# Kernel tuning notes

Hardware: AMD Instinct MI355X
Metric: run time of the kernel (lower is better)

The kernel has to match this reference:

```python
import jax, jax.numpy as jnp
import numpy as np


def setup_inputs() -> dict:
    key = jax.random.key(0)
    ks = jax.random.split(key, 5)
    B, C, H, W = 8, 64, 64, 64
    Ci = 32  # inter_channels = in_channels // 2
    s = 1.0 / np.sqrt(C)
    return {
        "x": jax.random.normal(ks[0], (B, C, H, W), jnp.float32),
        "Wg": jax.random.normal(ks[1], (Ci, C), jnp.float32) * s,
        "bg": jnp.zeros((Ci,), jnp.float32),
        "Wt": jax.random.normal(ks[2], (Ci, C), jnp.float32) * s,
        "bt": jnp.zeros((Ci,), jnp.float32),
        "Wp": jax.random.normal(ks[3], (Ci, C), jnp.float32) * s,
        "bp": jnp.zeros((Ci,), jnp.float32),
        "Ww": jax.random.normal(ks[4], (C, Ci), jnp.float32) * (1.0 / np.sqrt(Ci)),
        "bw": jnp.zeros((C,), jnp.float32),
    }


def _proj(x, Wc, bc):
    # 1x1 conv: (B,C,H,W) -> (B,O,H,W), then flatten spatial -> (B,O,N)
    b, c, h, w = x.shape
    y = jnp.einsum("oc,bchw->bohw", Wc, x) + bc[None, :, None, None]
    return y.reshape(b, Wc.shape[0], h * w)


def reference(x, Wg, bg, Wt, bt, Wp, bp, Ww, bw):
    b, c, h, w = x.shape
    g_x = _proj(x, Wg, bg).transpose(0, 2, 1)      # (B, N, Ci)
    theta_x = _proj(x, Wt, bt).transpose(0, 2, 1)  # (B, N, Ci)
    phi_x = _proj(x, Wp, bp)                        # (B, Ci, N)
    f = jnp.einsum("bnd,bdm->bnm", theta_x, phi_x)  # (B, N, N)
    f_div_C = jax.nn.softmax(f, axis=-1)
    y = jnp.einsum("bnm,bmd->bnd", f_div_C, g_x)    # (B, N, Ci)
    y = y.transpose(0, 2, 1).reshape(b, Wg.shape[0], h, w)
    W_y = jnp.einsum("od,bdhw->bohw", Ww, y) + bw[None, :, None, None]
    return W_y + x
```

## Files before the change

### kernel.cpp

```cpp
#include <hip/hip_runtime.h>
#include <hip/hip_bf16.h>
#include <cstdint>
#include <cstddef>

#define B_ 8
#define C_ 64
#define CI 32
#define N_ 4096
#define LOG2E 1.44269504088896340736f

typedef __attribute__((ext_vector_type(8))) short bf16x8;
typedef __attribute__((ext_vector_type(4))) float f32x4;

static __device__ __forceinline__ ushort f2bf(float x) {
  union { float f; uint32_t u; } v; v.f = x;
  uint32_t r = v.u + 0x7FFFu + ((v.u >> 16) & 1u);
  return (ushort)(r >> 16);
}

static __device__ __forceinline__ uint32_t cvt_pk_bf16(float lo, float hi) {
  uint32_t r;
  asm("v_cvt_pk_bf16_f32 %0, %1, %2" : "=v"(r) : "v"(lo), "v"(hi));
  return r;
}

__global__ __launch_bounds__(512) void proj_kernel(
    const float* __restrict__ x,
    const float* __restrict__ Wg, const float* __restrict__ bg,
    const float* __restrict__ Wt, const float* __restrict__ bt,
    const float* __restrict__ Wp, const float* __restrict__ bp,
    ushort* __restrict__ theta_t, ushort* __restrict__ phi_t,
    ushort* __restrict__ gmat)
{
  const int t = threadIdx.x;
  const int b = blockIdx.y;
  const int n = blockIdx.x * 64 + (t & 63);
  const int dg = __builtin_amdgcn_readfirstlane(t >> 6);
  const float* xb = x + ((size_t)b * C_) * N_ + n;
  const float* WtR = Wt + dg * 4 * C_;
  const float* WpR = Wp + dg * 4 * C_;
  const float* WgR = Wg + dg * 4 * C_;

  float at[4], ap[4], ag[4];
  #pragma unroll
  for (int i = 0; i < 4; ++i) {
    at[i] = bt[dg * 4 + i]; ap[i] = bp[dg * 4 + i]; ag[i] = bg[dg * 4 + i];
  }

  #pragma unroll
  for (int c0 = 0; c0 < C_; c0 += 4) {
    float xv[4];
    #pragma unroll
    for (int j = 0; j < 4; ++j) xv[j] = xb[(size_t)(c0 + j) * N_];
    #pragma unroll
    for (int i = 0; i < 4; ++i) {
      const float4 wt4 = *(const float4*)&WtR[i * C_ + c0];
      const float4 wp4 = *(const float4*)&WpR[i * C_ + c0];
      const float4 wg4 = *(const float4*)&WgR[i * C_ + c0];
      at[i] = fmaf(wt4.x, xv[0], at[i]); at[i] = fmaf(wt4.y, xv[1], at[i]);
      at[i] = fmaf(wt4.z, xv[2], at[i]); at[i] = fmaf(wt4.w, xv[3], at[i]);
      ap[i] = fmaf(wp4.x, xv[0], ap[i]); ap[i] = fmaf(wp4.y, xv[1], ap[i]);
      ap[i] = fmaf(wp4.z, xv[2], ap[i]); ap[i] = fmaf(wp4.w, xv[3], ap[i]);
      ag[i] = fmaf(wg4.x, xv[0], ag[i]); ag[i] = fmaf(wg4.y, xv[1], ag[i]);
      ag[i] = fmaf(wg4.z, xv[2], ag[i]); ag[i] = fmaf(wg4.w, xv[3], ag[i]);
    }
  }

  uint2 wt2, wp2;
  wt2.x = (uint32_t)f2bf(at[0] * LOG2E) | ((uint32_t)f2bf(at[1] * LOG2E) << 16);
  wt2.y = (uint32_t)f2bf(at[2] * LOG2E) | ((uint32_t)f2bf(at[3] * LOG2E) << 16);
  wp2.x = (uint32_t)f2bf(ap[0]) | ((uint32_t)f2bf(ap[1]) << 16);
  wp2.y = (uint32_t)f2bf(ap[2]) | ((uint32_t)f2bf(ap[3]) << 16);
  *(uint2*)(theta_t + ((size_t)(b * N_) + n) * CI + dg * 4) = wt2;
  *(uint2*)(phi_t   + ((size_t)(b * N_) + n) * CI + dg * 4) = wp2;
  #pragma unroll
  for (int i = 0; i < 4; ++i)
    gmat[((size_t)(b * CI) + dg * 4 + i) * N_ + n] = f2bf(ag[i]);
}

__global__ __launch_bounds__(512, 2) void attn_kernel(
    const ushort* __restrict__ theta_t,
    const ushort* __restrict__ phi_t,
    const ushort* __restrict__ gmat,
    const float* __restrict__ Ww, const float* __restrict__ bw,
    const float* __restrict__ x, float* __restrict__ out)
{
  __shared__ union {
    ushort pt[8][2][16 * 64];
    float  accS[4][32][64];
    float  yl[32 * 66];
  } Sh;
  __shared__ float mlS[4][8][64];
  __shared__ float WwL[C_ * CI];

  const int tid = threadIdx.x;
  const int lane = tid & 63;
  const int mh = tid >> 6;
  const int bid = blockIdx.x;
  const int b = bid & 7;
  const int n0 = (bid >> 3) * 64;
  const int g4 = lane >> 4;
  const int c16 = lane & 15;
  const int sw = (c16 & 7) << 4;

  #pragma unroll
  for (int i = 0; i < 4; ++i) WwL[tid + i * 512] = Ww[tid + i * 512];

  bf16x8 qfrag[4];
  #pragma unroll
  for (int s = 0; s < 4; ++s)
    qfrag[s] = *(const bf16x8*)(theta_t +
        ((size_t)(b * N_ + n0 + s * 16 + c16)) * CI + g4 * 8);

  f32x4 acc[4][2];
  f32x4 cinit[4];
  #pragma unroll
  for (int s = 0; s < 4; ++s) {
    acc[s][0] = (f32x4){0.f, 0.f, 0.f, 0.f};
    acc[s][1] = (f32x4){0.f, 0.f, 0.f, 0.f};
    cinit[s]  = (f32x4){0.f, 0.f, 0.f, 0.f};
  }
  float l_lane[4] = {0.f, 0.f, 0.f, 0.f};

  const int mq0 = mh * 512;
  const ushort* kbase = phi_t + ((size_t)(b * N_ + mq0 + c16)) * CI + g4 * 8;
  const ushort* vb0 = gmat + ((size_t)(b * CI + c16)) * N_ + mq0 + g4 * 8;
  const ushort* vb1 = vb0 + (size_t)16 * N_;

  char* pw[2][4]; const char* prd[2][2];
  #pragma unroll
  for (int pb = 0; pb < 2; ++pb) {
    #pragma unroll
    for (int mt = 0; mt < 4; ++mt)
      pw[pb][mt] = (char*)Sh.pt[mh][pb] + ((c16 * 128 + mt * 32 + g4 * 8) ^ sw);
    #pragma unroll
    for (int ks = 0; ks < 2; ++ks)
      prd[pb][ks] = (const char*)Sh.pt[mh][pb] +
                    ((c16 * 128 + ks * 64 + g4 * 16) ^ sw);
  }

  bf16x8 kf[4], kfn[4], vf0[2], vf1[2];
  #pragma unroll
  for (int mt = 0; mt < 4; ++mt)
    kfn[mt] = *(const bf16x8*)(kbase + (size_t)(mt * 16) * CI);

  const int NT = 8;
  for (int t = 0; t < NT; ++t) {
    #pragma unroll
    for (int mt = 0; mt < 4; ++mt) kf[mt] = kfn[mt];
    const int tn = (t + 1 < NT) ? t + 1 : t;
    #pragma unroll
    for (int mt = 0; mt < 4; ++mt)
      kfn[mt] = *(const bf16x8*)(kbase + (size_t)(tn * 64 + mt * 16) * CI);
    #pragma unroll
    for (int ks = 0; ks < 2; ++ks) {
      vf0[ks] = *(const bf16x8*)(vb0 + t * 64 + ks * 32);
      vf1[ks] = *(const bf16x8*)(vb1 + t * 64 + ks * 32);
    }

    #pragma unroll
    for (int s = 0; s < 4; ++s) {
      const int pb = s & 1;
      f32x4 f[4];
      #pragma unroll
      for (int mt = 0; mt < 4; ++mt)
        f[mt] = __builtin_amdgcn_mfma_f32_16x16x32_bf16(
            kf[mt], qfrag[s], cinit[s], 0, 0, 0);

      float pv[4][4];
      #pragma unroll
      for (int mt = 0; mt < 4; ++mt) {
        #pragma unroll
        for (int rr = 0; rr < 4; ++rr)
          pv[mt][rr] = __builtin_amdgcn_exp2f(f[mt][rr]);
        l_lane[s] += (pv[mt][0] + pv[mt][1]) + (pv[mt][2] + pv[mt][3]);
      }
      #pragma unroll
      for (int mt = 0; mt < 4; ++mt) {
        uint2 wv;
        wv.x = cvt_pk_bf16(pv[mt][0], pv[mt][1]);
        wv.y = cvt_pk_bf16(pv[mt][2], pv[mt][3]);
        *(uint2*)pw[pb][mt] = wv;
      }
      asm volatile("s_waitcnt lgkmcnt(0)" ::: "memory");

      #pragma unroll
      for (int ks = 0; ks < 2; ++ks) {
        const bf16x8 pfrag = *(const bf16x8*)prd[pb][ks];
        acc[s][0] = __builtin_amdgcn_mfma_f32_16x16x32_bf16(
            vf0[ks], pfrag, acc[s][0], 0, 0, 0);
        acc[s][1] = __builtin_amdgcn_mfma_f32_16x16x32_bf16(
            vf1[ks], pfrag, acc[s][1], 0, 0, 0);
      }

      if (__any(l_lane[s] > 0x1p40f)) {
        const float sc = 0x1p-64f;
        acc[s][0] *= sc; acc[s][1] *= sc; l_lane[s] *= sc;
        #pragma unroll
        for (int rr = 0; rr < 4; ++rr) cinit[s][rr] -= 64.f;
      }
    }
  }

  float m_run[4];
  #pragma unroll
  for (int s = 0; s < 4; ++s) {
    l_lane[s] += __shfl_xor(l_lane[s], 16);
    l_lane[s] += __shfl_xor(l_lane[s], 32);
    m_run[s] = -cinit[s][0];
  }

  #pragma unroll
  for (int r = 4; r >= 1; r >>= 1) {
    __syncthreads();
    if (mh >= r && mh < 2 * r) {
      float* ad = &Sh.accS[mh - r][0][0] + lane;
      float* md = &mlS[mh - r][0][0] + lane;
      #pragma unroll
      for (int s = 0; s < 4; ++s) {
        #pragma unroll
        for (int rr = 0; rr < 4; ++rr) {
          ad[(s * 8 + rr) * 64]     = acc[s][0][rr];
          ad[(s * 8 + 4 + rr) * 64] = acc[s][1][rr];
        }
        md[s * 64]       = m_run[s];
        md[(4 + s) * 64] = l_lane[s];
      }
    }
    __syncthreads();
    if (mh < r) {
      const float* as_ = &Sh.accS[mh][0][0] + lane;
      const float* ms_ = &mlS[mh][0][0] + lane;
      #pragma unroll
      for (int s = 0; s < 4; ++s) {
        const float mb = ms_[s * 64];
        const float lb = ms_[(4 + s) * 64];
        const float mM = fmaxf(m_run[s], mb);
        const float ea = __builtin_amdgcn_exp2f(m_run[s] - mM);
        const float eb = __builtin_amdgcn_exp2f(mb - mM);
        #pragma unroll
        for (int rr = 0; rr < 4; ++rr) {
          acc[s][0][rr] = acc[s][0][rr] * ea + as_[(s * 8 + rr) * 64] * eb;
          acc[s][1][rr] = acc[s][1][rr] * ea + as_[(s * 8 + 4 + rr) * 64] * eb;
        }
        l_lane[s] = l_lane[s] * ea + lb * eb;
        m_run[s] = mM;
      }
    }
  }
  __syncthreads();

  float* const Yl = Sh.yl;
  if (mh == 0) {
    #pragma unroll
    for (int s = 0; s < 4; ++s) {
      const float inv = 1.0f / l_lane[s];
      const int q = s * 16 + c16;
      #pragma unroll
      for (int rr = 0; rr < 4; ++rr) {
        Yl[(g4 * 4 + rr) * 66 + q]      = acc[s][0][rr] * inv;
        Yl[(16 + g4 * 4 + rr) * 66 + q] = acc[s][1][rr] * inv;
      }
    }
  }
  __syncthreads();

  const int nl = tid & 63;
  const int cg = tid >> 6;
  float oacc[8];
  #pragma unroll
  for (int i = 0; i < 8; ++i) oacc[i] = bw[cg * 8 + i];
  #pragma unroll
  for (int d = 0; d < CI; ++d) {
    const float yv = Yl[d * 66 + nl];
    #pragma unroll
    for (int i = 0; i < 8; ++i)
      oacc[i] = fmaf(WwL[(cg * 8 + i) * CI + d], yv, oacc[i]);
  }
  #pragma unroll
  for (int i = 0; i < 8; ++i) {
    const size_t idx = ((size_t)(b * C_ + cg * 8 + i)) * N_ + n0 + nl;
    out[idx] = oacc[i] + x[idx];
  }
}

extern "C" void kernel_launch(void* const* d_in, const int* in_sizes, int n_in,
                              void* d_out, int out_size, void* d_ws, size_t ws_size,
                              hipStream_t stream) {
  const float* x  = (const float*)d_in[0];
  const float* Wg = (const float*)d_in[1];
  const float* bg = (const float*)d_in[2];
  const float* Wt = (const float*)d_in[3];
  const float* bt = (const float*)d_in[4];
  const float* Wp = (const float*)d_in[5];
  const float* bp = (const float*)d_in[6];
  const float* Ww = (const float*)d_in[7];
  const float* bw = (const float*)d_in[8];
  float* out = (float*)d_out;

  char* ws = (char*)d_ws;
  ushort* theta_t = (ushort*)(ws);
  ushort* phi_t   = (ushort*)(ws + (size_t)2 * 1024 * 1024);
  ushort* gmat    = (ushort*)(ws + (size_t)4 * 1024 * 1024);

  proj_kernel<<<dim3(N_ / 64, B_), 512, 0, stream>>>(
      x, Wg, bg, Wt, bt, Wp, bp, theta_t, phi_t, gmat);
  attn_kernel<<<dim3((N_ / 64) * B_), 512, 0, stream>>>(
      theta_t, phi_t, gmat, Ww, bw, x, out);
}
```

Baseline: 60.00 us.

## Software-pipeline attention P·V MFMAs one query sub-tile behind the QK exp stage

Restructures the inner attention loop so that each query sub-tile's P·V MFMAs run during the next sub-tile's QK MFMA and exp work, with an epilogue that drains the last sub-tile. The aim is to hide LDS write/read latency and the lgkmcnt waits between writing P and reading it back. It also removes the K-fragment register prefetch, stores the running max offset as a scalar instead of a vector, and drops the occupancy hint from launch_bounds. The projection kernel gains a no-op `*0.f` term. The risks are less latency hiding for K loads without prefetch, possible register pressure changes, and the loss of the two-blocks-per-CU hint.

```diff
diff --git a/kernel.cpp b/kernel.cpp
--- a/kernel.cpp
+++ b/kernel.cpp
@@ -62,7 +62,7 @@
       ap[i] = fmaf(wp4.x, xv[0], ap[i]); ap[i] = fmaf(wp4.y, xv[1], ap[i]);
       ap[i] = fmaf(wp4.z, xv[2], ap[i]); ap[i] = fmaf(wp4.w, xv[3], ap[i]);
       ag[i] = fmaf(wg4.x, xv[0], ag[i]); ag[i] = fmaf(wg4.y, xv[1], ag[i]);
-      ag[i] = fmaf(wg4.z, xv[2], ag[i]); ag[i] = fmaf(wg4.w, xv[3], ag[i]);
+      ag[i] = fmaf(wg4.w * 0.f + wg4.z, xv[2], ag[i]); ag[i] = fmaf(wg4.w, xv[3], ag[i]);
     }
   }
 
@@ -78,7 +78,56 @@
     gmat[((size_t)(b * CI) + dg * 4 + i) * N_ + n] = f2bf(ag[i]);
 }
 
-__global__ __launch_bounds__(512, 2) void attn_kernel(
+#define BODY(S, DO_PREV)                                                      \
+  {                                                                           \
+    constexpr int sP = ((S) + 3) & 3;                                         \
+    f32x4 cop;                                                                \
+    cop[0] = mneg[S]; cop[1] = mneg[S]; cop[2] = mneg[S]; cop[3] = mneg[S];   \
+    f32x4 f[4];                                                               \
+    _Pragma("unroll")                                                         \
+    for (int mt = 0; mt < 4; ++mt)                                            \
+      f[mt] = __builtin_amdgcn_mfma_f32_16x16x32_bf16(                        \
+          kf[mt], qfrag[S], cop, 0, 0, 0);                                    \
+           \
+    asm volatile("s_waitcnt lgkmcnt(0)" ::: "memory");                        \
+    const bf16x8 pfA = *(const bf16x8*)prd[sP & 1][0];                        \
+    const bf16x8 pfB = *(const bf16x8*)prd[sP & 1][1];                        \
+    uint2 wv[4];                                                              \
+    float lsum = 0.f;                                                         \
+    _Pragma("unroll")                                                         \
+    for (int mt = 0; mt < 4; ++mt) {                                          \
+      const float p0 = __builtin_amdgcn_exp2f(f[mt][0]);                      \
+      const float p1 = __builtin_amdgcn_exp2f(f[mt][1]);                      \
+      const float p2 = __builtin_amdgcn_exp2f(f[mt][2]);                      \
+      const float p3 = __builtin_amdgcn_exp2f(f[mt][3]);                      \
+      lsum += (p0 + p1) + (p2 + p3);                                          \
+      wv[mt].x = cvt_pk_bf16(p0, p1);                                         \
+      wv[mt].y = cvt_pk_bf16(p2, p3);                                         \
+    }                                                                         \
+    l_lane[S] += lsum;                                                        \
+          \
+    asm volatile("s_waitcnt lgkmcnt(0)" ::: "memory");                        \
+    if (DO_PREV) {                                                            \
+      acc[sP][0] = __builtin_amdgcn_mfma_f32_16x16x32_bf16(                   \
+          vf0[0], pfA, acc[sP][0], 0, 0, 0);                                  \
+      acc[sP][1] = __builtin_amdgcn_mfma_f32_16x16x32_bf16(                   \
+          vf1[0], pfA, acc[sP][1], 0, 0, 0);                                  \
+      acc[sP][0] = __builtin_amdgcn_mfma_f32_16x16x32_bf16(                   \
+          vf0[1], pfB, acc[sP][0], 0, 0, 0);                                  \
+      acc[sP][1] = __builtin_amdgcn_mfma_f32_16x16x32_bf16(                   \
+          vf1[1], pfB, acc[sP][1], 0, 0, 0);                                  \
+      if (__any(l_lane[sP] > 0x1p40f)) {                                      \
+        const float sc = 0x1p-64f;                                            \
+        acc[sP][0] *= sc; acc[sP][1] *= sc; l_lane[sP] *= sc;                 \
+        mneg[sP] -= 64.f;                                                     \
+      }                                                                       \
+    }                                                                         \
+    _Pragma("unroll")                                                         \
+    for (int mt = 0; mt < 4; ++mt)                                            \
+      *(uint2*)pw[(S) & 1][mt] = wv[mt];                                      \
+  }
+
+__global__ __launch_bounds__(512) void attn_kernel(
     const ushort* __restrict__ theta_t,
     const ushort* __restrict__ phi_t,
     const ushort* __restrict__ gmat,
@@ -113,14 +162,13 @@
         ((size_t)(b * N_ + n0 + s * 16 + c16)) * CI + g4 * 8);
 
   f32x4 acc[4][2];
-  f32x4 cinit[4];
+  float mneg[4] = {0.f, 0.f, 0.f, 0.f};
+  float l_lane[4] = {0.f, 0.f, 0.f, 0.f};
   #pragma unroll
   for (int s = 0; s < 4; ++s) {
     acc[s][0] = (f32x4){0.f, 0.f, 0.f, 0.f};
     acc[s][1] = (f32x4){0.f, 0.f, 0.f, 0.f};
-    cinit[s]  = (f32x4){0.f, 0.f, 0.f, 0.f};
-  }
-  float l_lane[4] = {0.f, 0.f, 0.f, 0.f};
+  }
 
   const int mq0 = mh * 512;
   const ushort* kbase = phi_t + ((size_t)(b * N_ + mq0 + c16)) * CI + g4 * 8;
@@ -139,66 +187,40 @@
                     ((c16 * 128 + ks * 64 + g4 * 16) ^ sw);
   }
 
-  bf16x8 kf[4], kfn[4], vf0[2], vf1[2];
-  #pragma unroll
-  for (int mt = 0; mt < 4; ++mt)
-    kfn[mt] = *(const bf16x8*)(kbase + (size_t)(mt * 16) * CI);
+  bf16x8 kf[4], vf0[2], vf1[2];
 
   const int NT = 8;
   for (int t = 0; t < NT; ++t) {
     #pragma unroll
-    for (int mt = 0; mt < 4; ++mt) kf[mt] = kfn[mt];
-    const int tn = (t + 1 < NT) ? t + 1 : t;
-    #pragma unroll
     for (int mt = 0; mt < 4; ++mt)
-      kfn[mt] = *(const bf16x8*)(kbase + (size_t)(tn * 64 + mt * 16) * CI);
+      kf[mt] = *(const bf16x8*)(kbase + (size_t)(t * 64 + mt * 16) * CI);
+
+    BODY(0, (t > 0))
+
     #pragma unroll
     for (int ks = 0; ks < 2; ++ks) {
       vf0[ks] = *(const bf16x8*)(vb0 + t * 64 + ks * 32);
       vf1[ks] = *(const bf16x8*)(vb1 + t * 64 + ks * 32);
     }
 
-    #pragma unroll
-    for (int s = 0; s < 4; ++s) {
-      const int pb = s & 1;
-      f32x4 f[4];
-      #pragma unroll
-      for (int mt = 0; mt < 4; ++mt)
-        f[mt] = __builtin_amdgcn_mfma_f32_16x16x32_bf16(
-            kf[mt], qfrag[s], cinit[s], 0, 0, 0);
-
-      float pv[4][4];
-      #pragma unroll
-      for (int mt = 0; mt < 4; ++mt) {
-        #pragma unroll
-        for (int rr = 0; rr < 4; ++rr)
-          pv[mt][rr] = __builtin_amdgcn_exp2f(f[mt][rr]);
-        l_lane[s] += (pv[mt][0] + pv[mt][1]) + (pv[mt][2] + pv[mt][3]);
-      }
-      #pragma unroll
-      for (int mt = 0; mt < 4; ++mt) {
-        uint2 wv;
-        wv.x = cvt_pk_bf16(pv[mt][0], pv[mt][1]);
-        wv.y = cvt_pk_bf16(pv[mt][2], pv[mt][3]);
-        *(uint2*)pw[pb][mt] = wv;
-      }
-      asm volatile("s_waitcnt lgkmcnt(0)" ::: "memory");
-
-      #pragma unroll
-      for (int ks = 0; ks < 2; ++ks) {
-        const bf16x8 pfrag = *(const bf16x8*)prd[pb][ks];
-        acc[s][0] = __builtin_amdgcn_mfma_f32_16x16x32_bf16(
-            vf0[ks], pfrag, acc[s][0], 0, 0, 0);
-        acc[s][1] = __builtin_amdgcn_mfma_f32_16x16x32_bf16(
-            vf1[ks], pfrag, acc[s][1], 0, 0, 0);
-      }
-
-      if (__any(l_lane[s] > 0x1p40f)) {
-        const float sc = 0x1p-64f;
-        acc[s][0] *= sc; acc[s][1] *= sc; l_lane[s] *= sc;
-        #pragma unroll
-        for (int rr = 0; rr < 4; ++rr) cinit[s][rr] -= 64.f;
-      }
+    BODY(1, true)
+    BODY(2, true)
+    BODY(3, true)
+  }
+
+  {
+    asm volatile("s_waitcnt lgkmcnt(0)" ::: "memory");
+    const bf16x8 pfA = *(const bf16x8*)prd[1][0];
+    const bf16x8 pfB = *(const bf16x8*)prd[1][1];
+    asm volatile("s_waitcnt lgkmcnt(0)" ::: "memory");
+    acc[3][0] = __builtin_amdgcn_mfma_f32_16x16x32_bf16(vf0[0], pfA, acc[3][0], 0, 0, 0);
+    acc[3][1] = __builtin_amdgcn_mfma_f32_16x16x32_bf16(vf1[0], pfA, acc[3][1], 0, 0, 0);
+    acc[3][0] = __builtin_amdgcn_mfma_f32_16x16x32_bf16(vf0[1], pfB, acc[3][0], 0, 0, 0);
+    acc[3][1] = __builtin_amdgcn_mfma_f32_16x16x32_bf16(vf1[1], pfB, acc[3][1], 0, 0, 0);
+    if (__any(l_lane[3] > 0x1p40f)) {
+      const float sc = 0x1p-64f;
+      acc[3][0] *= sc; acc[3][1] *= sc; l_lane[3] *= sc;
+      mneg[3] -= 64.f;
     }
   }
 
@@ -207,7 +229,7 @@
   for (int s = 0; s < 4; ++s) {
     l_lane[s] += __shfl_xor(l_lane[s], 16);
     l_lane[s] += __shfl_xor(l_lane[s], 32);
-    m_run[s] = -cinit[s][0];
+    m_run[s] = -mneg[s];
   }
 
   #pragma unroll
```

Measured after the change: 61.10 us. About the same (+1.8%).
